# Performance work log

Measured on AMD Instinct MI355X. Metric: run time of the kernel, lower is better.

The kernel has to match this reference:

```python
import jax, jax.numpy as jnp
import numpy as np


def setup_inputs() -> dict:
    key = jax.random.key(0)
    k_x, k_B, k_C, k_D, k_step = jax.random.split(key, 5)
    Bsz, L, H = 8, 4096, 512
    P = 256  # effective state dim = dim_ssm_state // 2 (conj_sym)
    # s4d_inv init for Lambda (complex, stored as real/imag parts)
    n = jnp.arange(P, dtype=jnp.float32)
    Lambda_re = -0.5 * jnp.ones((P,), dtype=jnp.float32)
    Lambda_im = (P / np.pi) * (P / (2.0 * n + 1.0) - 1.0)
    # lecun_normal-ish init for B (P,H,2) and C (H,P,2), divided by sqrt(2)
    B = jax.random.normal(k_B, (P, H, 2), dtype=jnp.float32) * (1.0 / np.sqrt(H)) / np.sqrt(2.0)
    C = jax.random.normal(k_C, (H, P, 2), dtype=jnp.float32) * (1.0 / np.sqrt(P)) / np.sqrt(2.0)
    D = jax.random.normal(k_D, (H,), dtype=jnp.float32)
    dt_min, dt_max = 1e-3, 1e-1
    log_step = jax.random.uniform(k_step, (P,)) * (np.log(dt_max) - np.log(dt_min)) + np.log(dt_min)
    x = jax.random.normal(k_x, (Bsz, L, H), dtype=jnp.float32)
    return {"x": x, "Lambda_re": Lambda_re, "Lambda_im": Lambda_im,
            "B": B, "C": C, "D": D, "log_step": log_step.astype(jnp.float32)}


def _binary_op(q_i, q_j):
    A_i, b_i = q_i
    A_j, b_j = q_j
    return (A_j * A_i, A_j * b_i + b_j)


def reference(x, Lambda_re, Lambda_im, B, C, D, log_step):
    # Assemble complex params (conj_sym=True)
    Lam = Lambda_re + 1j * Lambda_im          # (P,)
    B_tilde = B[..., 0] + 1j * B[..., 1]      # (P,H)
    C_tilde = C[..., 0] + 1j * C[..., 1]      # (H,P)
    step = jnp.exp(log_step)                  # (P,) step_rescale = 1.0
    # ZOH discretization
    Lambda_bar = jnp.exp(Lam * step)                              # (P,)
    B_bar = ((Lambda_bar - 1.0) / Lam)[:, None] * B_tilde         # (P,H)
    # Bu elements: (Bsz, L, P) complex
    Bu = jnp.einsum('blh,ph->blp', x.astype(B_bar.dtype), B_bar)
    Lam_elems = jnp.broadcast_to(Lambda_bar, Bu.shape)
    # Parallel linear recurrence over time axis
    _, xs = jax.lax.associative_scan(_binary_op, (Lam_elems, Bu), axis=1)
    # Output projection with conjugate symmetry + D skip
    ys = 2.0 * jnp.einsum('blp,hp->blh', xs, C_tilde).real + D * x
    return ys
```

## Files before the change

kernel.cpp:

```cpp
#include <hip/hip_runtime.h>
#include <hip/hip_bf16.h>
#include <hip/hip_fp16.h>
#include <math.h>

#define BSZ 8
#define LSEQ 4096
#define HDIM 512
#define PDIM 256
#define MROWS (BSZ * LSEQ)
#define NDIM 512
#define CHUNK 64
#define NCHUNK (LSEQ / CHUNK)

typedef __attribute__((ext_vector_type(8))) short bf16x8;
typedef __attribute__((ext_vector_type(4))) float f32x4;

__global__ __launch_bounds__(256) void convert_x(const float* __restrict__ x,
                                                 __hip_bfloat16* __restrict__ xb,
                                                 int n4) {
    int i = blockIdx.x * blockDim.x + threadIdx.x;
    if (i >= n4) return;
    float4 v = ((const float4*)x)[i];
    union { ushort4 u; __hip_bfloat16 h[4]; } o;
    o.h[0] = __float2bfloat16(v.x);
    o.h[1] = __float2bfloat16(v.y);
    o.h[2] = __float2bfloat16(v.z);
    o.h[3] = __float2bfloat16(v.w);
    ((ushort4*)xb)[i] = o.u;
}

__global__ void precompute_w1(const float* __restrict__ Lre,
                              const float* __restrict__ Lim,
                              const float* __restrict__ logstep,
                              const float* __restrict__ Bmat,
                              __hip_bfloat16* __restrict__ W1T,
                              float* __restrict__ a_re,
                              float* __restrict__ a_im) {
    int idx = blockIdx.x * blockDim.x + threadIdx.x;
    if (idx >= PDIM * HDIM) return;
    int p = idx / HDIM, h = idx % HDIM;
    double step = exp((double)logstep[p]);
    double dlr = (double)Lre[p], dli = (double)Lim[p];
    double mag = exp(dlr * step);
    double ar = mag * cos(dli * step);
    double ai = mag * sin(dli * step);
    double den = dlr * dlr + dli * dli;
    double nr = ar - 1.0, ni = ai;
    double fr = (nr * dlr + ni * dli) / den;
    double fi = (ni * dlr - nr * dli) / den;
    double br = (double)Bmat[(size_t)(p * HDIM + h) * 2 + 0];
    double bi = (double)Bmat[(size_t)(p * HDIM + h) * 2 + 1];
    W1T[(size_t)(2 * p) * HDIM + h]     = __float2bfloat16((float)(fr * br - fi * bi));
    W1T[(size_t)(2 * p + 1) * HDIM + h] = __float2bfloat16((float)(fr * bi + fi * br));
    if (h == 0) { a_re[p] = (float)ar; a_im[p] = (float)ai; }
}

__global__ void precompute_w2(const float* __restrict__ Cmat,
                              __hip_bfloat16* __restrict__ W2T) {
    int idx = blockIdx.x * blockDim.x + threadIdx.x;
    if (idx >= HDIM * PDIM) return;
    int h = idx / PDIM, p = idx % PDIM;
    float cr = Cmat[(size_t)(h * PDIM + p) * 2 + 0];
    float ci = Cmat[(size_t)(h * PDIM + p) * 2 + 1];
    W2T[(size_t)h * NDIM + 2 * p]     = __float2bfloat16(2.0f * cr);
    W2T[(size_t)h * NDIM + 2 * p + 1] = __float2bfloat16(-2.0f * ci);
}

template <typename OT, bool SKIP>
__global__ __launch_bounds__(256) void gemm_bt(
    const __hip_bfloat16* __restrict__ A,
    const __hip_bfloat16* __restrict__ BT,
    OT* __restrict__ C,
    const float* __restrict__ Dvec,
    const __hip_bfloat16* __restrict__ Xskip,
    int M, int N, int K) {
    __shared__ __hip_bfloat16 smA[64 * 32];
    __shared__ __hip_bfloat16 smB[128 * 32];

    const int tid = threadIdx.x;
    const int lane = tid & 63;
    const int wave = tid >> 6;
    const int row0 = blockIdx.y * 64;
    const int col0 = blockIdx.x * 128;
    const int wm = (wave >> 1) * 32;
    const int wn = (wave & 1) * 64;

    const int sr = lane >> 2;
    const int sk = (lane & 3) * 8;
    const int quad = lane >> 4;
    const int l15 = lane & 15;

    f32x4 acc[2][4] = {};

    for (int k0 = 0; k0 < K; k0 += 32) {
        {
            const int chunk = wave * 16;
            const __hip_bfloat16* gA = A + (size_t)(row0 + chunk + sr) * K + k0 + sk;
            __builtin_amdgcn_global_load_lds(
                (const __attribute__((address_space(1))) void*)gA,
                (__attribute__((address_space(3))) void*)&smA[chunk * 32], 16, 0, 0);
        }
#pragma unroll
        for (int q = 0; q < 2; ++q) {
            const int chunk = wave * 32 + q * 16;
            const __hip_bfloat16* gB = BT + (size_t)(col0 + chunk + sr) * K + k0 + sk;
            __builtin_amdgcn_global_load_lds(
                (const __attribute__((address_space(1))) void*)gB,
                (__attribute__((address_space(3))) void*)&smB[chunk * 32], 16, 0, 0);
        }
        __syncthreads();

        bf16x8 af[2], bfr[4];
#pragma unroll
        for (int i = 0; i < 2; ++i)
            af[i] = *(const bf16x8*)&smA[(wm + i * 16 + l15) * 32 + quad * 8];
#pragma unroll
        for (int j = 0; j < 4; ++j)
            bfr[j] = *(const bf16x8*)&smB[(wn + j * 16 + l15) * 32 + quad * 8];
#pragma unroll
        for (int i = 0; i < 2; ++i)
#pragma unroll
            for (int j = 0; j < 4; ++j)
                acc[i][j] = __builtin_amdgcn_mfma_f32_16x16x32_bf16(
                    af[i], bfr[j], acc[i][j], 0, 0, 0);
        __syncthreads();
    }

#pragma unroll
    for (int i = 0; i < 2; ++i) {
        const int mbase = row0 + wm + i * 16 + quad * 4;
#pragma unroll
        for (int j = 0; j < 4; ++j) {
            const int col = col0 + wn + j * 16 + l15;
            const float dv = SKIP ? Dvec[col] : 0.0f;
#pragma unroll
            for (int r = 0; r < 4; ++r) {
                const size_t m = (size_t)(mbase + r);
                float v = acc[i][j][r];
                if (SKIP) v += dv * __bfloat162float(Xskip[m * N + col]);
                if constexpr (sizeof(OT) == 2) {
                    C[m * N + col] = OT(v);
                } else {
                    C[m * N + col] = v;
                }
            }
        }
    }
}

__global__ __launch_bounds__(256) void scan_chunks(const __half2* __restrict__ Bu2,
                                                   const float* __restrict__ a_re,
                                                   const float* __restrict__ a_im,
                                                   float2* __restrict__ S) {
    int b = blockIdx.x / NCHUNK;
    int c = blockIdx.x % NCHUNK;
    int p = threadIdx.x;
    float ar = a_re[p], ai = a_im[p];
    float sr = 0.0f, si = 0.0f;
    size_t m0 = (size_t)b * LSEQ + (size_t)c * CHUNK;
    for (int j = 0; j < CHUNK; ++j) {
        float2 u = __half22float2(Bu2[(m0 + j) * PDIM + p]);
        float nsr = ar * sr - ai * si + u.x;
        float nsi = ar * si + ai * sr + u.y;
        sr = nsr; si = nsi;
    }
    S[(size_t)(b * NCHUNK + c) * PDIM + p] = make_float2(sr, si);
}

__global__ __launch_bounds__(256) void scan_carry(const float2* __restrict__ S,
                                                  const float* __restrict__ a_re,
                                                  const float* __restrict__ a_im,
                                                  float2* __restrict__ carry) {
    int b = blockIdx.x;
    int p = threadIdx.x;
    double ar = (double)a_re[p], ai = (double)a_im[p];
#pragma unroll
    for (int i = 0; i < 6; ++i) {
        double nr = ar * ar - ai * ai;
        double ni = 2.0 * ar * ai;
        ar = nr; ai = ni;
    }
    float alr = (float)ar, ali = (float)ai;
    float cr = 0.0f, ci = 0.0f;
    for (int c = 0; c < NCHUNK; ++c) {
        carry[(size_t)(b * NCHUNK + c) * PDIM + p] = make_float2(cr, ci);
        float2 s = S[(size_t)(b * NCHUNK + c) * PDIM + p];
        float ncr = alr * cr - ali * ci + s.x;
        float nci = alr * ci + ali * cr + s.y;
        cr = ncr; ci = nci;
    }
}

__global__ __launch_bounds__(256) void scan_apply(const __half2* __restrict__ Bu2,
                                                  const float* __restrict__ a_re,
                                                  const float* __restrict__ a_im,
                                                  const float2* __restrict__ carry,
                                                  ushort2* __restrict__ xsb2) {
    int b = blockIdx.x / NCHUNK;
    int c = blockIdx.x % NCHUNK;
    int p = threadIdx.x;
    float ar = a_re[p], ai = a_im[p];
    float2 c0 = carry[(size_t)(b * NCHUNK + c) * PDIM + p];
    float sr = c0.x, si = c0.y;
    size_t m0 = (size_t)b * LSEQ + (size_t)c * CHUNK;
    for (int j = 0; j < CHUNK; ++j) {
        size_t idx = (m0 + j) * PDIM + p;
        float2 u = __half22float2(Bu2[idx]);
        float nsr = ar * sr - ai * si + u.x;
        float nsi = ar * si + ai * sr + u.y;
        sr = nsr; si = nsi;
        union { ushort2 u2; __hip_bfloat16 h[2]; } o;
        o.h[0] = __float2bfloat16(sr);
        o.h[1] = __float2bfloat16(si);
        xsb2[idx] = o.u2;
    }
}

extern "C" void kernel_launch(void* const* d_in, const int* in_sizes, int n_in,
                              void* d_out, int out_size, void* d_ws, size_t ws_size,
                              hipStream_t stream) {
    const float* x       = (const float*)d_in[0];
    const float* Lre     = (const float*)d_in[1];
    const float* Lim     = (const float*)d_in[2];
    const float* Bmat    = (const float*)d_in[3];
    const float* Cmat    = (const float*)d_in[4];
    const float* Dvec    = (const float*)d_in[5];
    const float* logstep = (const float*)d_in[6];
    float* out = (float*)d_out;

    char* ws = (char*)d_ws;
    const size_t MB = 1u << 20;
    __hip_bfloat16* xb  = (__hip_bfloat16*)(ws + 0);
    __hip_bfloat16* xsb = (__hip_bfloat16*)(ws + 32 * MB);
    __half* Bu          = (__half*)(ws + 64 * MB);
    __hip_bfloat16* W1T = (__hip_bfloat16*)(ws + 96 * MB);
    __hip_bfloat16* W2T = (__hip_bfloat16*)(ws + 96 * MB + 512 * 1024);
    float*  a_re  = (float*)(ws + 97 * MB);
    float*  a_im  = (float*)(ws + 97 * MB + 4096);
    float2* S     = (float2*)(ws + 98 * MB);
    float2* carry = (float2*)(ws + 99 * MB);

    convert_x<<<(MROWS * HDIM / 4 + 255) / 256, 256, 0, stream>>>(
        x, xb, MROWS * HDIM / 4);
    precompute_w1<<<(PDIM * HDIM + 255) / 256, 256, 0, stream>>>(
        Lre, Lim, logstep, Bmat, W1T, a_re, a_im);
    precompute_w2<<<(HDIM * PDIM + 255) / 256, 256, 0, stream>>>(Cmat, W2T);

    dim3 ggrid(NDIM / 128, MROWS / 64);
    gemm_bt<__half, false><<<ggrid, 256, 0, stream>>>(
        xb, W1T, Bu, nullptr, nullptr, MROWS, NDIM, HDIM);

    scan_chunks<<<BSZ * NCHUNK, 256, 0, stream>>>((const __half2*)Bu, a_re, a_im, S);
    scan_carry<<<BSZ, 256, 0, stream>>>(S, a_re, a_im, carry);
    scan_apply<<<BSZ * NCHUNK, 256, 0, stream>>>((const __half2*)Bu, a_re, a_im,
                                                 carry, (ushort2*)xsb);

    gemm_bt<float, true><<<ggrid, 256, 0, stream>>>(
        xsb, W2T, out, Dvec, xb, MROWS, HDIM, NDIM);
}
```

Measured before the change: 226.1 us.

## Shrink GEMM tiles to 64x64 and vectorize scan kernels over four states per thread

The GEMM tile drops from 64x128 to 64x64, which doubles the grid and halves per-wave accumulators. This trades more blocks and occupancy for less operand reuse. The chunk-scan and apply kernels now give each thread four consecutive state channels, using 16-byte loads and stores, and each block covers four chunks. This means fewer blocks but wider memory accesses. The carry kernel batches eight loads of chunk sums ahead of the serial recurrence to expose memory-level parallelism.

```diff
diff --git a/kernel.cpp b/kernel.cpp
--- a/kernel.cpp
+++ b/kernel.cpp
@@ -75,52 +75,45 @@
     const __hip_bfloat16* __restrict__ Xskip,
     int M, int N, int K) {
     __shared__ __hip_bfloat16 smA[64 * 32];
-    __shared__ __hip_bfloat16 smB[128 * 32];
+    __shared__ __hip_bfloat16 smB[64 * 32];
 
     const int tid = threadIdx.x;
     const int lane = tid & 63;
     const int wave = tid >> 6;
     const int row0 = blockIdx.y * 64;
-    const int col0 = blockIdx.x * 128;
+    const int col0 = blockIdx.x * 64;
     const int wm = (wave >> 1) * 32;
-    const int wn = (wave & 1) * 64;
+    const int wn = (wave & 1) * 32;
 
     const int sr = lane >> 2;
     const int sk = (lane & 3) * 8;
     const int quad = lane >> 4;
     const int l15 = lane & 15;
 
-    f32x4 acc[2][4] = {};
+    f32x4 acc[2][2] = {};
 
     for (int k0 = 0; k0 < K; k0 += 32) {
-        {
-            const int chunk = wave * 16;
-            const __hip_bfloat16* gA = A + (size_t)(row0 + chunk + sr) * K + k0 + sk;
-            __builtin_amdgcn_global_load_lds(
-                (const __attribute__((address_space(1))) void*)gA,
-                (__attribute__((address_space(3))) void*)&smA[chunk * 32], 16, 0, 0);
-        }
-#pragma unroll
-        for (int q = 0; q < 2; ++q) {
-            const int chunk = wave * 32 + q * 16;
-            const __hip_bfloat16* gB = BT + (size_t)(col0 + chunk + sr) * K + k0 + sk;
-            __builtin_amdgcn_global_load_lds(
-                (const __attribute__((address_space(1))) void*)gB,
-                (__attribute__((address_space(3))) void*)&smB[chunk * 32], 16, 0, 0);
-        }
+        const int chunk = wave * 16;
+        const __hip_bfloat16* gA = A + (size_t)(row0 + chunk + sr) * K + k0 + sk;
+        const __hip_bfloat16* gB = BT + (size_t)(col0 + chunk + sr) * K + k0 + sk;
+        __builtin_amdgcn_global_load_lds(
+            (const __attribute__((address_space(1))) void*)gA,
+            (__attribute__((address_space(3))) void*)&smA[chunk * 32], 16, 0, 0);
+        __builtin_amdgcn_global_load_lds(
+            (const __attribute__((address_space(1))) void*)gB,
+            (__attribute__((address_space(3))) void*)&smB[chunk * 32], 16, 0, 0);
         __syncthreads();
 
-        bf16x8 af[2], bfr[4];
+        bf16x8 af[2], bfr[2];
+#pragma unroll
+        for (int i = 0; i < 2; ++i) {
+            af[i]  = *(const bf16x8*)&smA[(wm + i * 16 + l15) * 32 + quad * 8];
+            bfr[i] = *(const bf16x8*)&smB[(wn + i * 16 + l15) * 32 + quad * 8];
+        }
 #pragma unroll
         for (int i = 0; i < 2; ++i)
-            af[i] = *(const bf16x8*)&smA[(wm + i * 16 + l15) * 32 + quad * 8];
-#pragma unroll
-        for (int j = 0; j < 4; ++j)
-            bfr[j] = *(const bf16x8*)&smB[(wn + j * 16 + l15) * 32 + quad * 8];
-#pragma unroll
-        for (int i = 0; i < 2; ++i)
-#pragma unroll
-            for (int j = 0; j < 4; ++j)
+#pragma unroll
+            for (int j = 0; j < 2; ++j)
                 acc[i][j] = __builtin_amdgcn_mfma_f32_16x16x32_bf16(
                     af[i], bfr[j], acc[i][j], 0, 0, 0);
         __syncthreads();
@@ -130,7 +123,7 @@
     for (int i = 0; i < 2; ++i) {
         const int mbase = row0 + wm + i * 16 + quad * 4;
 #pragma unroll
-        for (int j = 0; j < 4; ++j) {
+        for (int j = 0; j < 2; ++j) {
             const int col = col0 + wn + j * 16 + l15;
             const float dv = SKIP ? Dvec[col] : 0.0f;
 #pragma unroll
@@ -152,27 +145,39 @@
                                                    const float* __restrict__ a_re,
                                                    const float* __restrict__ a_im,
                                                    float2* __restrict__ S) {
-    int b = blockIdx.x / NCHUNK;
-    int c = blockIdx.x % NCHUNK;
-    int p = threadIdx.x;
-    float ar = a_re[p], ai = a_im[p];
-    float sr = 0.0f, si = 0.0f;
-    size_t m0 = (size_t)b * LSEQ + (size_t)c * CHUNK;
+    const int b = blockIdx.x >> 4;
+    const int cq = blockIdx.x & 15;
+    const int g = threadIdx.x >> 6;
+    const int c = cq * 4 + g;
+    const int pb = (threadIdx.x & 63) * 4;
+    float4 arv = *(const float4*)&a_re[pb];
+    float4 aiv = *(const float4*)&a_im[pb];
+    const float ar[4] = {arv.x, arv.y, arv.z, arv.w};
+    const float ai[4] = {aiv.x, aiv.y, aiv.z, aiv.w};
+    float sr[4] = {}, si[4] = {};
+    const size_t m0 = (size_t)b * LSEQ + (size_t)c * CHUNK;
     for (int j = 0; j < CHUNK; ++j) {
-        float2 u = __half22float2(Bu2[(m0 + j) * PDIM + p]);
-        float nsr = ar * sr - ai * si + u.x;
-        float nsi = ar * si + ai * sr + u.y;
-        sr = nsr; si = nsi;
-    }
-    S[(size_t)(b * NCHUNK + c) * PDIM + p] = make_float2(sr, si);
+        union { float4 f; __half2 h[4]; } u;
+        u.f = *(const float4*)&Bu2[(m0 + j) * PDIM + pb];
+#pragma unroll
+        for (int k = 0; k < 4; ++k) {
+            float2 v = __half22float2(u.h[k]);
+            float nsr = ar[k] * sr[k] - ai[k] * si[k] + v.x;
+            float nsi = ar[k] * si[k] + ai[k] * sr[k] + v.y;
+            sr[k] = nsr; si[k] = nsi;
+        }
+    }
+    float2* sp = &S[(size_t)(b * NCHUNK + c) * PDIM + pb];
+#pragma unroll
+    for (int k = 0; k < 4; ++k) sp[k] = make_float2(sr[k], si[k]);
 }
 
 __global__ __launch_bounds__(256) void scan_carry(const float2* __restrict__ S,
                                                   const float* __restrict__ a_re,
                                                   const float* __restrict__ a_im,
                                                   float2* __restrict__ carry) {
-    int b = blockIdx.x;
-    int p = threadIdx.x;
+    const int b = blockIdx.x;
+    const int p = threadIdx.x;
     double ar = (double)a_re[p], ai = (double)a_im[p];
 #pragma unroll
     for (int i = 0; i < 6; ++i) {
@@ -180,14 +185,20 @@
         double ni = 2.0 * ar * ai;
         ar = nr; ai = ni;
     }
-    float alr = (float)ar, ali = (float)ai;
+    const float alr = (float)ar, ali = (float)ai;
     float cr = 0.0f, ci = 0.0f;
-    for (int c = 0; c < NCHUNK; ++c) {
-        carry[(size_t)(b * NCHUNK + c) * PDIM + p] = make_float2(cr, ci);
-        float2 s = S[(size_t)(b * NCHUNK + c) * PDIM + p];
-        float ncr = alr * cr - ali * ci + s.x;
-        float nci = alr * ci + ali * cr + s.y;
-        cr = ncr; ci = nci;
+    for (int cg = 0; cg < NCHUNK / 8; ++cg) {
+        float2 sv[8];
+#pragma unroll
+        for (int t = 0; t < 8; ++t)
+            sv[t] = S[(size_t)(b * NCHUNK + cg * 8 + t) * PDIM + p];
+#pragma unroll
+        for (int t = 0; t < 8; ++t) {
+            carry[(size_t)(b * NCHUNK + cg * 8 + t) * PDIM + p] = make_float2(cr, ci);
+            float ncr = alr * cr - ali * ci + sv[t].x;
+            float nci = alr * ci + ali * cr + sv[t].y;
+            cr = ncr; ci = nci;
+        }
     }
 }
 
@@ -196,23 +207,35 @@
                                                   const float* __restrict__ a_im,
                                                   const float2* __restrict__ carry,
                                                   ushort2* __restrict__ xsb2) {
-    int b = blockIdx.x / NCHUNK;
-    int c = blockIdx.x % NCHUNK;
-    int p = threadIdx.x;
-    float ar = a_re[p], ai = a_im[p];
-    float2 c0 = carry[(size_t)(b * NCHUNK + c) * PDIM + p];
-    float sr = c0.x, si = c0.y;
-    size_t m0 = (size_t)b * LSEQ + (size_t)c * CHUNK;
+    const int b = blockIdx.x >> 4;
+    const int cq = blockIdx.x & 15;
+    const int g = threadIdx.x >> 6;
+    const int c = cq * 4 + g;
+    const int pb = (threadIdx.x & 63) * 4;
+    float4 arv = *(const float4*)&a_re[pb];
+    float4 aiv = *(const float4*)&a_im[pb];
+    const float ar[4] = {arv.x, arv.y, arv.z, arv.w};
+    const float ai[4] = {aiv.x, aiv.y, aiv.z, aiv.w};
+    float sr[4], si[4];
+    const float2* cp = &carry[(size_t)(b * NCHUNK + c) * PDIM + pb];
+#pragma unroll
+    for (int k = 0; k < 4; ++k) { float2 c0 = cp[k]; sr[k] = c0.x; si[k] = c0.y; }
+    const size_t m0 = (size_t)b * LSEQ + (size_t)c * CHUNK;
     for (int j = 0; j < CHUNK; ++j) {
-        size_t idx = (m0 + j) * PDIM + p;
-        float2 u = __half22float2(Bu2[idx]);
-        float nsr = ar * sr - ai * si + u.x;
-        float nsi = ar * si + ai * sr + u.y;
-        sr = nsr; si = nsi;
-        union { ushort2 u2; __hip_bfloat16 h[2]; } o;
-        o.h[0] = __float2bfloat16(sr);
-        o.h[1] = __float2bfloat16(si);
-        xsb2[idx] = o.u2;
+        const size_t idx = (m0 + j) * PDIM + pb;
+        union { float4 f; __half2 h[4]; } u;
+        u.f = *(const float4*)&Bu2[idx];
+        union { ushort4 o4[2]; __hip_bfloat16 hb[8]; } o;
+#pragma unroll
+        for (int k = 0; k < 4; ++k) {
+            float2 v = __half22float2(u.h[k]);
+            float nsr = ar[k] * sr[k] - ai[k] * si[k] + v.x;
+            float nsi = ar[k] * si[k] + ai[k] * sr[k] + v.y;
+            sr[k] = nsr; si[k] = nsi;
+            o.hb[2 * k]     = __float2bfloat16(nsr);
+            o.hb[2 * k + 1] = __float2bfloat16(nsi);
+        }
+        *(float4*)&xsb2[idx] = *(float4*)&o.o4[0];
     }
 }
 
@@ -246,15 +269,17 @@
         Lre, Lim, logstep, Bmat, W1T, a_re, a_im);
     precompute_w2<<<(HDIM * PDIM + 255) / 256, 256, 0, stream>>>(Cmat, W2T);
 
-    dim3 ggrid(NDIM / 128, MROWS / 64);
-    gemm_bt<__half, false><<<ggrid, 256, 0, stream>>>(
+    dim3 ggrid1(NDIM / 64, MROWS / 64);
+    gemm_bt<__half, false><<<ggrid1, 256, 0, stream>>>(
         xb, W1T, Bu, nullptr, nullptr, MROWS, NDIM, HDIM);
 
-    scan_chunks<<<BSZ * NCHUNK, 256, 0, stream>>>((const __half2*)Bu, a_re, a_im, S);
+    scan_chunks<<<BSZ * NCHUNK / 4, 256, 0, stream>>>(
+        (const __half2*)Bu, a_re, a_im, S);
     scan_carry<<<BSZ, 256, 0, stream>>>(S, a_re, a_im, carry);
-    scan_apply<<<BSZ * NCHUNK, 256, 0, stream>>>((const __half2*)Bu, a_re, a_im,
-                                                 carry, (ushort2*)xsb);
-
-    gemm_bt<float, true><<<ggrid, 256, 0, stream>>>(
+    scan_apply<<<BSZ * NCHUNK / 4, 256, 0, stream>>>(
+        (const __half2*)Bu, a_re, a_im, carry, (ushort2*)xsb);
+
+    dim3 ggrid2(HDIM / 64, MROWS / 64);
+    gemm_bt<float, true><<<ggrid2, 256, 0, stream>>>(
         xsb, W2T, out, Dvec, xb, MROWS, HDIM, NDIM);
 }
```

Result: slower. 264.1 us (+16.8%).

## Fuse x conversion and intra-chunk scan into first GEMM, apply carry via precomputed powers

Applied to the files above, without the earlier changes.

The first GEMM now reads fp32 x directly and converts it to bf16 in registers, so the separate conversion kernel is gone. It also stages its output tile in shared memory and runs the within-chunk recurrence there, writing local scan states and per-chunk sums. A new apply kernel adds carry times precomputed powers of Lambda in parallel, replacing the sequential rescan over Bu. This removes one full pass over the intermediate and the bf16 copy of x. In exchange, the in-GEMM scan runs on only 64 threads per block, and the second GEMM reads the fp32 skip input.

```diff
diff --git a/kernel.cpp b/kernel.cpp
--- a/kernel.cpp
+++ b/kernel.cpp
@@ -14,20 +14,6 @@
 
 typedef __attribute__((ext_vector_type(8))) short bf16x8;
 typedef __attribute__((ext_vector_type(4))) float f32x4;
-
-__global__ __launch_bounds__(256) void convert_x(const float* __restrict__ x,
-                                                 __hip_bfloat16* __restrict__ xb,
-                                                 int n4) {
-    int i = blockIdx.x * blockDim.x + threadIdx.x;
-    if (i >= n4) return;
-    float4 v = ((const float4*)x)[i];
-    union { ushort4 u; __hip_bfloat16 h[4]; } o;
-    o.h[0] = __float2bfloat16(v.x);
-    o.h[1] = __float2bfloat16(v.y);
-    o.h[2] = __float2bfloat16(v.z);
-    o.h[3] = __float2bfloat16(v.w);
-    ((ushort4*)xb)[i] = o.u;
-}
 
 __global__ void precompute_w1(const float* __restrict__ Lre,
                               const float* __restrict__ Lim,
@@ -66,16 +52,30 @@
     W2T[(size_t)h * NDIM + 2 * p + 1] = __float2bfloat16(-2.0f * ci);
 }
 
-template <typename OT, bool SKIP>
-__global__ __launch_bounds__(256) void gemm_bt(
-    const __hip_bfloat16* __restrict__ A,
+__global__ void precompute_pow(const float* __restrict__ a_re,
+                               const float* __restrict__ a_im,
+                               float2* __restrict__ apow) {
+    const int p = threadIdx.x;
+    const float ar = a_re[p], ai = a_im[p];
+    float cr = ar, ci = ai;
+    for (int j = 0; j < CHUNK; ++j) {
+        apow[j * PDIM + p] = make_float2(cr, ci);
+        float nr = cr * ar - ci * ai;
+        float ni = cr * ai + ci * ar;
+        cr = nr; ci = ni;
+    }
+}
+
+__global__ __launch_bounds__(256) void gemm1_scan(
+    const float* __restrict__ x,
     const __hip_bfloat16* __restrict__ BT,
-    OT* __restrict__ C,
-    const float* __restrict__ Dvec,
-    const __hip_bfloat16* __restrict__ Xskip,
-    int M, int N, int K) {
+    const float* __restrict__ a_re,
+    const float* __restrict__ a_im,
+    __half2* __restrict__ local2,
+    float2* __restrict__ S) {
     __shared__ __hip_bfloat16 smA[64 * 32];
     __shared__ __hip_bfloat16 smB[128 * 32];
+    __shared__ float stile[64 * 132];
 
     const int tid = threadIdx.x;
     const int lane = tid & 63;
@@ -92,18 +92,23 @@
 
     f32x4 acc[2][4] = {};
 
-    for (int k0 = 0; k0 < K; k0 += 32) {
+    for (int k0 = 0; k0 < 512; k0 += 32) {
         {
-            const int chunk = wave * 16;
-            const __hip_bfloat16* gA = A + (size_t)(row0 + chunk + sr) * K + k0 + sk;
-            __builtin_amdgcn_global_load_lds(
-                (const __attribute__((address_space(1))) void*)gA,
-                (__attribute__((address_space(3))) void*)&smA[chunk * 32], 16, 0, 0);
+            const int arow = wave * 16 + sr;
+            const float* gx = &x[(size_t)(row0 + arow) * 512 + k0 + sk];
+            float4 v0 = *(const float4*)gx;
+            float4 v1 = *(const float4*)(gx + 4);
+            union { bf16x8 v; __hip_bfloat16 h[8]; } o;
+            o.h[0] = __float2bfloat16(v0.x); o.h[1] = __float2bfloat16(v0.y);
+            o.h[2] = __float2bfloat16(v0.z); o.h[3] = __float2bfloat16(v0.w);
+            o.h[4] = __float2bfloat16(v1.x); o.h[5] = __float2bfloat16(v1.y);
+            o.h[6] = __float2bfloat16(v1.z); o.h[7] = __float2bfloat16(v1.w);
+            *(bf16x8*)&smA[arow * 32 + sk] = o.v;
         }
 #pragma unroll
         for (int q = 0; q < 2; ++q) {
             const int chunk = wave * 32 + q * 16;
-            const __hip_bfloat16* gB = BT + (size_t)(col0 + chunk + sr) * K + k0 + sk;
+            const __hip_bfloat16* gB = BT + (size_t)(col0 + chunk + sr) * 512 + k0 + sk;
             __builtin_amdgcn_global_load_lds(
                 (const __attribute__((address_space(1))) void*)gB,
                 (__attribute__((address_space(3))) void*)&smB[chunk * 32], 16, 0, 0);
@@ -128,51 +133,39 @@
 
 #pragma unroll
     for (int i = 0; i < 2; ++i) {
-        const int mbase = row0 + wm + i * 16 + quad * 4;
+        const int rbase = wm + i * 16 + quad * 4;
 #pragma unroll
         for (int j = 0; j < 4; ++j) {
-            const int col = col0 + wn + j * 16 + l15;
-            const float dv = SKIP ? Dvec[col] : 0.0f;
-#pragma unroll
-            for (int r = 0; r < 4; ++r) {
-                const size_t m = (size_t)(mbase + r);
-                float v = acc[i][j][r];
-                if (SKIP) v += dv * __bfloat162float(Xskip[m * N + col]);
-                if constexpr (sizeof(OT) == 2) {
-                    C[m * N + col] = OT(v);
-                } else {
-                    C[m * N + col] = v;
-                }
-            }
-        }
-    }
-}
-
-__global__ __launch_bounds__(256) void scan_chunks(const __half2* __restrict__ Bu2,
-                                                   const float* __restrict__ a_re,
-                                                   const float* __restrict__ a_im,
-                                                   float2* __restrict__ S) {
-    int b = blockIdx.x / NCHUNK;
-    int c = blockIdx.x % NCHUNK;
-    int p = threadIdx.x;
-    float ar = a_re[p], ai = a_im[p];
-    float sr = 0.0f, si = 0.0f;
-    size_t m0 = (size_t)b * LSEQ + (size_t)c * CHUNK;
-    for (int j = 0; j < CHUNK; ++j) {
-        float2 u = __half22float2(Bu2[(m0 + j) * PDIM + p]);
-        float nsr = ar * sr - ai * si + u.x;
-        float nsi = ar * si + ai * sr + u.y;
-        sr = nsr; si = nsi;
-    }
-    S[(size_t)(b * NCHUNK + c) * PDIM + p] = make_float2(sr, si);
+            const int col = wn + j * 16 + l15;
+#pragma unroll
+            for (int r = 0; r < 4; ++r)
+                stile[(rbase + r) * 132 + col] = acc[i][j][r];
+        }
+    }
+    __syncthreads();
+
+    if (tid < 64) {
+        const int pg = blockIdx.x * 64 + tid;
+        const float ar = a_re[pg], ai = a_im[pg];
+        float sr_ = 0.0f, si_ = 0.0f;
+        const size_t mbase = (size_t)row0 * PDIM + pg;
+        for (int j = 0; j < CHUNK; ++j) {
+            float2 u = *(const float2*)&stile[j * 132 + 2 * tid];
+            float nsr = ar * sr_ - ai * si_ + u.x;
+            float nsi = ar * si_ + ai * sr_ + u.y;
+            sr_ = nsr; si_ = nsi;
+            local2[mbase + (size_t)j * PDIM] = __float22half2_rn(make_float2(nsr, nsi));
+        }
+        S[(size_t)blockIdx.y * PDIM + pg] = make_float2(sr_, si_);
+    }
 }
 
 __global__ __launch_bounds__(256) void scan_carry(const float2* __restrict__ S,
                                                   const float* __restrict__ a_re,
                                                   const float* __restrict__ a_im,
                                                   float2* __restrict__ carry) {
-    int b = blockIdx.x;
-    int p = threadIdx.x;
+    const int b = blockIdx.x;
+    const int p = threadIdx.x;
     double ar = (double)a_re[p], ai = (double)a_im[p];
 #pragma unroll
     for (int i = 0; i < 6; ++i) {
@@ -180,39 +173,133 @@
         double ni = 2.0 * ar * ai;
         ar = nr; ai = ni;
     }
-    float alr = (float)ar, ali = (float)ai;
+    const float alr = (float)ar, ali = (float)ai;
     float cr = 0.0f, ci = 0.0f;
-    for (int c = 0; c < NCHUNK; ++c) {
-        carry[(size_t)(b * NCHUNK + c) * PDIM + p] = make_float2(cr, ci);
-        float2 s = S[(size_t)(b * NCHUNK + c) * PDIM + p];
-        float ncr = alr * cr - ali * ci + s.x;
-        float nci = alr * ci + ali * cr + s.y;
-        cr = ncr; ci = nci;
-    }
-}
-
-__global__ __launch_bounds__(256) void scan_apply(const __half2* __restrict__ Bu2,
-                                                  const float* __restrict__ a_re,
-                                                  const float* __restrict__ a_im,
-                                                  const float2* __restrict__ carry,
-                                                  ushort2* __restrict__ xsb2) {
-    int b = blockIdx.x / NCHUNK;
-    int c = blockIdx.x % NCHUNK;
-    int p = threadIdx.x;
-    float ar = a_re[p], ai = a_im[p];
-    float2 c0 = carry[(size_t)(b * NCHUNK + c) * PDIM + p];
-    float sr = c0.x, si = c0.y;
-    size_t m0 = (size_t)b * LSEQ + (size_t)c * CHUNK;
-    for (int j = 0; j < CHUNK; ++j) {
-        size_t idx = (m0 + j) * PDIM + p;
-        float2 u = __half22float2(Bu2[idx]);
-        float nsr = ar * sr - ai * si + u.x;
-        float nsi = ar * si + ai * sr + u.y;
-        sr = nsr; si = nsi;
-        union { ushort2 u2; __hip_bfloat16 h[2]; } o;
-        o.h[0] = __float2bfloat16(sr);
-        o.h[1] = __float2bfloat16(si);
-        xsb2[idx] = o.u2;
+    for (int cg = 0; cg < NCHUNK / 8; ++cg) {
+        float2 sv[8];
+#pragma unroll
+        for (int t = 0; t < 8; ++t)
+            sv[t] = S[(size_t)(b * NCHUNK + cg * 8 + t) * PDIM + p];
+#pragma unroll
+        for (int t = 0; t < 8; ++t) {
+            carry[(size_t)(b * NCHUNK + cg * 8 + t) * PDIM + p] = make_float2(cr, ci);
+            float ncr = alr * cr - ali * ci + sv[t].x;
+            float nci = alr * ci + ali * cr + sv[t].y;
+            cr = ncr; ci = nci;
+        }
+    }
+}
+
+__global__ __launch_bounds__(256) void apply_carry(
+    const __half2* __restrict__ local2,
+    const float2* __restrict__ apow,
+    const float2* __restrict__ carry,
+    ushort2* __restrict__ xsb2) {
+    const int bc = blockIdx.x;
+    const int slot = threadIdx.x & 63;
+    const int rgrp = threadIdx.x >> 6;
+
+    float2 cv[4];
+    {
+        float4 c01 = *(const float4*)&carry[(size_t)bc * PDIM + slot * 4];
+        float4 c23 = *(const float4*)&carry[(size_t)bc * PDIM + slot * 4 + 2];
+        cv[0] = make_float2(c01.x, c01.y); cv[1] = make_float2(c01.z, c01.w);
+        cv[2] = make_float2(c23.x, c23.y); cv[3] = make_float2(c23.z, c23.w);
+    }
+
+    for (int jg = 0; jg < CHUNK / 4; ++jg) {
+        const int j = jg * 4 + rgrp;
+        const size_t m = (size_t)bc * CHUNK + j;
+        union { float4 f; __half2 h[4]; } u;
+        u.f = ((const float4*)local2)[m * 64 + slot];
+        float4 p01 = *(const float4*)&apow[j * PDIM + slot * 4];
+        float4 p23 = *(const float4*)&apow[j * PDIM + slot * 4 + 2];
+        const float2 pw[4] = {make_float2(p01.x, p01.y), make_float2(p01.z, p01.w),
+                              make_float2(p23.x, p23.y), make_float2(p23.z, p23.w)};
+        union { ushort4 o4[2]; __hip_bfloat16 hb[8]; } o;
+#pragma unroll
+        for (int k = 0; k < 4; ++k) {
+            float2 v = __half22float2(u.h[k]);
+            float re = v.x + pw[k].x * cv[k].x - pw[k].y * cv[k].y;
+            float im = v.y + pw[k].x * cv[k].y + pw[k].y * cv[k].x;
+            o.hb[2 * k]     = __float2bfloat16(re);
+            o.hb[2 * k + 1] = __float2bfloat16(im);
+        }
+        *(float4*)&xsb2[m * PDIM + slot * 4] = *(float4*)&o.o4[0];
+    }
+}
+
+__global__ __launch_bounds__(256) void gemm2(
+    const __hip_bfloat16* __restrict__ A,
+    const __hip_bfloat16* __restrict__ BT,
+    float* __restrict__ C,
+    const float* __restrict__ Dvec,
+    const float* __restrict__ Xskip) {
+    __shared__ __hip_bfloat16 smA[64 * 32];
+    __shared__ __hip_bfloat16 smB[128 * 32];
+
+    const int tid = threadIdx.x;
+    const int lane = tid & 63;
+    const int wave = tid >> 6;
+    const int row0 = blockIdx.y * 64;
+    const int col0 = blockIdx.x * 128;
+    const int wm = (wave >> 1) * 32;
+    const int wn = (wave & 1) * 64;
+
+    const int sr = lane >> 2;
+    const int sk = (lane & 3) * 8;
+    const int quad = lane >> 4;
+    const int l15 = lane & 15;
+
+    f32x4 acc[2][4] = {};
+
+    for (int k0 = 0; k0 < 512; k0 += 32) {
+        {
+            const int chunk = wave * 16;
+            const __hip_bfloat16* gA = A + (size_t)(row0 + chunk + sr) * 512 + k0 + sk;
+            __builtin_amdgcn_global_load_lds(
+                (const __attribute__((address_space(1))) void*)gA,
+                (__attribute__((address_space(3))) void*)&smA[chunk * 32], 16, 0, 0);
+        }
+#pragma unroll
+        for (int q = 0; q < 2; ++q) {
+            const int chunk = wave * 32 + q * 16;
+            const __hip_bfloat16* gB = BT + (size_t)(col0 + chunk + sr) * 512 + k0 + sk;
+            __builtin_amdgcn_global_load_lds(
+                (const __attribute__((address_space(1))) void*)gB,
+                (__attribute__((address_space(3))) void*)&smB[chunk * 32], 16, 0, 0);
+        }
+        __syncthreads();
+
+        bf16x8 af[2], bfr[4];
+#pragma unroll
+        for (int i = 0; i < 2; ++i)
+            af[i] = *(const bf16x8*)&smA[(wm + i * 16 + l15) * 32 + quad * 8];
+#pragma unroll
+        for (int j = 0; j < 4; ++j)
+            bfr[j] = *(const bf16x8*)&smB[(wn + j * 16 + l15) * 32 + quad * 8];
+#pragma unroll
+        for (int i = 0; i < 2; ++i)
+#pragma unroll
+            for (int j = 0; j < 4; ++j)
+                acc[i][j] = __builtin_amdgcn_mfma_f32_16x16x32_bf16(
+                    af[i], bfr[j], acc[i][j], 0, 0, 0);
+        __syncthreads();
+    }
+
+#pragma unroll
+    for (int i = 0; i < 2; ++i) {
+        const int mbase = row0 + wm + i * 16 + quad * 4;
+#pragma unroll
+        for (int j = 0; j < 4; ++j) {
+            const int col = col0 + wn + j * 16 + l15;
+            const float dv = Dvec[col];
+#pragma unroll
+            for (int r = 0; r < 4; ++r) {
+                const size_t m = (size_t)(mbase + r);
+                C[m * 512 + col] = acc[i][j][r] + dv * Xskip[m * 512 + col];
+            }
+        }
     }
 }
 
@@ -230,31 +317,28 @@
 
     char* ws = (char*)d_ws;
     const size_t MB = 1u << 20;
-    __hip_bfloat16* xb  = (__hip_bfloat16*)(ws + 0);
-    __hip_bfloat16* xsb = (__hip_bfloat16*)(ws + 32 * MB);
-    __half* Bu          = (__half*)(ws + 64 * MB);
-    __hip_bfloat16* W1T = (__hip_bfloat16*)(ws + 96 * MB);
-    __hip_bfloat16* W2T = (__hip_bfloat16*)(ws + 96 * MB + 512 * 1024);
-    float*  a_re  = (float*)(ws + 97 * MB);
-    float*  a_im  = (float*)(ws + 97 * MB + 4096);
-    float2* S     = (float2*)(ws + 98 * MB);
-    float2* carry = (float2*)(ws + 99 * MB);
-
-    convert_x<<<(MROWS * HDIM / 4 + 255) / 256, 256, 0, stream>>>(
-        x, xb, MROWS * HDIM / 4);
+    __half2* local2     = (__half2*)(ws + 0);
+    ushort2* xsb2       = (ushort2*)(ws + 32 * MB);
+    __hip_bfloat16* W1T = (__hip_bfloat16*)(ws + 64 * MB);
+    __hip_bfloat16* W2T = (__hip_bfloat16*)(ws + 64 * MB + 512 * 1024);
+    float*  a_re  = (float*)(ws + 65 * MB);
+    float*  a_im  = (float*)(ws + 65 * MB + 4096);
+    float2* apow  = (float2*)(ws + 66 * MB);
+    float2* S     = (float2*)(ws + 67 * MB);
+    float2* carry = (float2*)(ws + 68 * MB);
+
     precompute_w1<<<(PDIM * HDIM + 255) / 256, 256, 0, stream>>>(
         Lre, Lim, logstep, Bmat, W1T, a_re, a_im);
     precompute_w2<<<(HDIM * PDIM + 255) / 256, 256, 0, stream>>>(Cmat, W2T);
-
-    dim3 ggrid(NDIM / 128, MROWS / 64);
-    gemm_bt<__half, false><<<ggrid, 256, 0, stream>>>(
-        xb, W1T, Bu, nullptr, nullptr, MROWS, NDIM, HDIM);
-
-    scan_chunks<<<BSZ * NCHUNK, 256, 0, stream>>>((const __half2*)Bu, a_re, a_im, S);
+    precompute_pow<<<1, 256, 0, stream>>>(a_re, a_im, apow);
+
+    dim3 g1(NDIM / 128, MROWS / 64);
+    gemm1_scan<<<g1, 256, 0, stream>>>(x, W1T, a_re, a_im, local2, S);
+
     scan_carry<<<BSZ, 256, 0, stream>>>(S, a_re, a_im, carry);
-    scan_apply<<<BSZ * NCHUNK, 256, 0, stream>>>((const __half2*)Bu, a_re, a_im,
-                                                 carry, (ushort2*)xsb);
-
-    gemm_bt<float, true><<<ggrid, 256, 0, stream>>>(
-        xsb, W2T, out, Dvec, xb, MROWS, HDIM, NDIM);
-}
+
+    apply_carry<<<BSZ * NCHUNK, 256, 0, stream>>>(local2, apow, carry, xsb2);
+
+    dim3 g2(HDIM / 128, MROWS / 64);
+    gemm2<<<g2, 256, 0, stream>>>((const __hip_bfloat16*)xsb2, W2T, out, Dvec, x);
+}
```

Measured after the change: 243.7 us. 1.08x slower.
